# Optimization experiments

Hardware: AMD Instinct MI355X
Metric: run time of the kernel (lower is better)

The kernel has to match this reference:

```python
import jax, jax.numpy as jnp
import numpy as np

N_HEADS = 8

def setup_inputs() -> dict:
    key = jax.random.key(0)
    ks = jax.random.split(key, 8)
    N, D, H = 20000, 16, 256
    scale = np.float32(0.02)
    return {
        "h": jax.random.normal(ks[0], (N, H), dtype=jnp.float32),
        "attention_mask": jnp.zeros((N,), dtype=jnp.float32),
        "neighbor_idx": jax.random.randint(ks[1], (N, D), 0, N, dtype=jnp.int32),
        "Wq": jax.random.normal(ks[2], (H, H), dtype=jnp.float32) * scale,
        "bq": jnp.zeros((H,), dtype=jnp.float32),
        "Wk": jax.random.normal(ks[3], (H, H), dtype=jnp.float32) * scale,
        "bk": jnp.zeros((H,), dtype=jnp.float32),
        "Wv": jax.random.normal(ks[4], (H, H), dtype=jnp.float32) * scale,
        "bv": jnp.zeros((H,), dtype=jnp.float32),
    }

def reference(h, attention_mask, neighbor_idx, Wq, bq, Wk, bk, Wv, bv):
    N, H = h.shape
    nh = N_HEADS
    dh = H // nh
    inv_sqrt_dh = np.float32(1.0 / np.sqrt(dh))
    # query from each node's own state: [N, nh, dh]
    q = (h @ Wq.T + bq).reshape(N, nh, dh)
    # gather neighbor mailbox: [N, D, H]
    nb = h[neighbor_idx]
    k = (nb @ Wk.T + bk).reshape(N, -1, nh, dh)  # [N, D, nh, dh]
    v = (nb @ Wv.T + bv).reshape(N, -1, nh, dh)
    # scores: [N, nh, D]
    scores = jnp.einsum('nhd,nkhd->nhk', q, k) * inv_sqrt_dh
    # additive mask gathered from source nodes, broadcast over heads
    scores = scores + attention_mask[neighbor_idx][:, None, :]
    probs = jax.nn.softmax(scores, axis=-1)
    # dropout prob = 0.0 (eval) -> identity
    ctx = jnp.einsum('nhk,nkhd->nhd', probs, v).reshape(N, H)
    return ctx
```

## Files before the change

### kernel.cpp

```cpp
#include <hip/hip_runtime.h>
#include <hip/hip_fp16.h>
#include <math.h>

#define HDIM 256
#define DNEIGH 16

typedef __attribute__((ext_vector_type(8))) short short8;
typedef __attribute__((ext_vector_type(4))) float f32x4;

static __device__ __forceinline__ unsigned short f2bf(float f) {
    unsigned int u = __float_as_uint(f);
    unsigned int r = (u + 0x7fffu + ((u >> 16) & 1u)) >> 16;
    return (unsigned short)r;
}
static __device__ __forceinline__ float bf_lo(unsigned int u) {
    return __uint_as_float(u << 16);
}
static __device__ __forceinline__ float bf_hi(unsigned int u) {
    return __uint_as_float(u & 0xffff0000u);
}

#if __has_builtin(__builtin_amdgcn_cvt_pk_fp8_f32)
static __device__ __forceinline__ unsigned char f2fp8(float v) {
    int pk = __builtin_amdgcn_cvt_pk_fp8_f32(v, v, 0, false);
    return (unsigned char)(pk & 0xff);
}
#else
static __device__ __forceinline__ unsigned char f2fp8(float v) {
    unsigned short h = __half_as_ushort(__float2half(v * (1.0f / 256.0f)));
    unsigned short mag = h & 0x7fffu;
    mag = (unsigned short)((mag + 0x40u) >> 7);
    if (mag > 0x7f) mag = 0x7f;
    return (unsigned char)(((h >> 8) & 0x80u) | mag);
}
#endif

#if __has_builtin(__builtin_amdgcn_cvt_f32_fp8)
#define FP8D(u, i) __builtin_amdgcn_cvt_f32_fp8((u), (i))
#else
static __device__ __forceinline__ float fp8_byte_dec(unsigned int b) {
    unsigned int hb = ((b & 0x80u) << 8) | ((b & 0x7fu) << 7);
    return __half2float(__ushort_as_half((unsigned short)hb)) * 256.0f;
}
#define FP8D(u, i) fp8_byte_dec(((u) >> ((i) * 8)) & 0xffu)
#endif

static __device__ __forceinline__ void async_copy16(const void* g, void* l) {
    __builtin_amdgcn_global_load_lds(
        (const __attribute__((address_space(1))) unsigned int*)g,
        (__attribute__((address_space(3))) unsigned int*)l, 16, 0, 0);
}

__global__ __launch_bounds__(256) void cvt_kernel(
    const float* __restrict__ h,
    const float* __restrict__ wq, const float* __restrict__ wk, const float* __restrict__ wv,
    unsigned short* __restrict__ hb,
    unsigned short* __restrict__ wqb, unsigned short* __restrict__ wkb, unsigned short* __restrict__ wvb,
    int nh4)
{
    int i = blockIdx.x * 256 + threadIdx.x;
    const int total = nh4 + 3 * 16384;
    if (i >= total) return;
    const float4* src; unsigned short* dst; int off;
    if (i < nh4) { src = (const float4*)h; dst = hb; off = i; }
    else {
        int j = i - nh4; int s = j >> 14; off = j & 16383;
        src = (s == 0) ? (const float4*)wq : (s == 1) ? (const float4*)wk : (const float4*)wv;
        dst = (s == 0) ? wqb : (s == 1) ? wkb : wvb;
    }
    float4 v = src[off];
    ushort4 o;
    o.x = f2bf(v.x); o.y = f2bf(v.y); o.z = f2bf(v.z); o.w = f2bf(v.w);
    *(ushort4*)&dst[off * 4] = o;
}

__global__ __launch_bounds__(256, 1) void qkv_mfma_kernel(
    const unsigned short* __restrict__ hb,
    const unsigned short* __restrict__ Wqb,
    const unsigned short* __restrict__ Wkb,
    const unsigned short* __restrict__ Wvb,
    const float* __restrict__ bq, const float* __restrict__ bk, const float* __restrict__ bv,
    unsigned short* __restrict__ Qb, unsigned char* __restrict__ K8,
    unsigned short* __restrict__ Vb,
    int N)
{
    __shared__ unsigned short Ws[128 * 256];
    __shared__ unsigned short As[2][64 * 256];

    const int t = threadIdx.x;
    const int lane = t & 63;
    const int wid = t >> 6;
    const int wo = wid >> 1;
    const int wn2 = wid & 1;
    const int o0 = blockIdx.y * 128;
    const int sel = o0 >> 8;
    const int wrow0 = o0 & 255;

    const unsigned short* __restrict__ W = (sel == 0) ? Wqb : (sel == 1) ? Wkb : Wvb;
    const float* __restrict__ bias = (sel == 0) ? bq : (sel == 1) ? bk : bv;

    const int ntiles = (N + 63) >> 6;
    const int BX = gridDim.x;

    const int p = lane & 31;
    const int rhalf = lane >> 5;

#pragma unroll
    for (int r = 0; r < 16; ++r) {
        int lr = wid * 32 + r * 2 + rhalf;
        int c = (p & ~7) | ((p ^ lr) & 7);
        const unsigned short* gp = &W[(size_t)(wrow0 + lr) * 256 + c * 8];
        async_copy16(gp, &Ws[(wid * 32 + r * 2) * 256]);
    }
    {
        int g0 = blockIdx.x * 64;
#pragma unroll
        for (int r = 0; r < 8; ++r) {
            int lr = wid * 16 + r * 2 + rhalf;
            int c = (p & ~7) | ((p ^ lr) & 7);
            const unsigned short* gp = &hb[(size_t)(g0 + lr) * 256 + c * 8];
            async_copy16(gp, &As[0][(wid * 16 + r * 2) * 256]);
        }
    }
    __syncthreads();

    short8 af[8][4];
#pragma unroll
    for (int ks = 0; ks < 8; ++ks)
#pragma unroll
        for (int i = 0; i < 4; ++i) {
            int m = wo * 64 + i * 16 + (lane & 15);
            int c = ks * 4 + (lane >> 4);
            int pos = (c & ~7) | ((c ^ m) & 7);
            af[ks][i] = *(const short8*)&Ws[m * 256 + pos * 8];
        }

    const float qscale = 0.17677669529663688f;

    int tile = blockIdx.x;
    for (int it = 0; tile < ntiles; ++it, tile += BX) {
        int cur = it & 1;
        int nxt = tile + BX;
        if (nxt < ntiles) {
            int g0 = nxt * 64;
#pragma unroll
            for (int r = 0; r < 8; ++r) {
                int lr = wid * 16 + r * 2 + rhalf;
                int c = (p & ~7) | ((p ^ lr) & 7);
                const unsigned short* gp = &hb[(size_t)(g0 + lr) * 256 + c * 8];
                async_copy16(gp, &As[cur ^ 1][(wid * 16 + r * 2) * 256]);
            }
        }

        f32x4 acc[4][2] = {};
#pragma unroll
        for (int ks = 0; ks < 8; ++ks) {
            short8 bf[2];
#pragma unroll
            for (int j = 0; j < 2; ++j) {
                int n = wn2 * 32 + j * 16 + (lane & 15);
                int c = ks * 4 + (lane >> 4);
                int pos = (c & ~7) | ((c ^ n) & 7);
                bf[j] = *(const short8*)&As[cur][n * 256 + pos * 8];
            }
#pragma unroll
            for (int i = 0; i < 4; ++i)
#pragma unroll
                for (int j = 0; j < 2; ++j)
                    acc[i][j] = __builtin_amdgcn_mfma_f32_16x16x32_bf16(af[ks][i], bf[j], acc[i][j], 0, 0, 0);
        }

        int nodeb = tile * 64;
#pragma unroll
        for (int i = 0; i < 4; ++i) {
            int ch = wrow0 + wo * 64 + i * 16 + (lane >> 4) * 4;
            float4 b4 = *(const float4*)&bias[ch];
#pragma unroll
            for (int j = 0; j < 2; ++j) {
                int node = nodeb + wn2 * 32 + j * 16 + (lane & 15);
                if (node < N) {
                    float v0 = acc[i][j][0] + b4.x;
                    float v1 = acc[i][j][1] + b4.y;
                    float v2 = acc[i][j][2] + b4.z;
                    float v3 = acc[i][j][3] + b4.w;
                    if (sel == 0) {
                        ushort4 o;
                        o.x = f2bf(v0 * qscale); o.y = f2bf(v1 * qscale);
                        o.z = f2bf(v2 * qscale); o.w = f2bf(v3 * qscale);
                        *(ushort4*)&Qb[(size_t)node * HDIM + ch] = o;
                    } else if (sel == 1) {
                        uchar4 o;
                        o.x = f2fp8(v0); o.y = f2fp8(v1); o.z = f2fp8(v2); o.w = f2fp8(v3);
                        *(uchar4*)&K8[(size_t)node * HDIM + ch] = o;
                    } else {
                        ushort4 o;
                        o.x = f2bf(v0); o.y = f2bf(v1); o.z = f2bf(v2); o.w = f2bf(v3);
                        *(ushort4*)&Vb[(size_t)node * HDIM + ch] = o;
                    }
                }
            }
        }
        __syncthreads();
    }
}

__global__ __launch_bounds__(256) void attn4_kernel(
    const unsigned short* __restrict__ Qb,
    const unsigned char* __restrict__ K8,
    const unsigned short* __restrict__ Vb,
    const float* __restrict__ mask,
    const int* __restrict__ nidx,
    float* __restrict__ out,
    int N)
{
    const int w = threadIdx.x >> 6;
    const int lane = threadIdx.x & 63;
    const int n = blockIdx.x * 4 + w;
    if (n >= N) return;

    int idl = nidx[(size_t)n * DNEIGH + (lane & 15)];
    float mskl = mask[idl];

    unsigned int kreg[DNEIGH];
    uint2 vreg[DNEIGH];
#pragma unroll
    for (int d = 0; d < DNEIGH; ++d) {
        int id = __builtin_amdgcn_readlane(idl, d);
        kreg[d] = *(const unsigned int*)&K8[(size_t)id * HDIM + lane * 4];
        vreg[d] = *(const uint2*)&Vb[(size_t)id * HDIM + lane * 4];
    }

    uint2 qu = *(const uint2*)&Qb[(size_t)n * HDIM + lane * 4];
    const float q0 = bf_lo(qu.x), q1 = bf_hi(qu.x);
    const float q2 = bf_lo(qu.y), q3 = bf_hi(qu.y);

    float e[DNEIGH];
    float s = 0.f;
#pragma unroll
    for (int d = 0; d < DNEIGH; ++d) {
        float pdot = q0 * FP8D(kreg[d], 0) + q1 * FP8D(kreg[d], 1)
                   + q2 * FP8D(kreg[d], 2) + q3 * FP8D(kreg[d], 3);
        pdot += __shfl_xor(pdot, 1);
        pdot += __shfl_xor(pdot, 2);
        pdot += __shfl_xor(pdot, 4);
        float mk = __int_as_float(__builtin_amdgcn_readlane(__float_as_int(mskl), d));
        e[d] = __expf(pdot + mk);
        s += e[d];
    }
    float rs = 1.f / s;

    float4 acc = make_float4(0.f, 0.f, 0.f, 0.f);
#pragma unroll
    for (int d = 0; d < DNEIGH; ++d) {
        float wgt = e[d] * rs;
        acc.x += wgt * bf_lo(vreg[d].x);
        acc.y += wgt * bf_hi(vreg[d].x);
        acc.z += wgt * bf_lo(vreg[d].y);
        acc.w += wgt * bf_hi(vreg[d].y);
    }
    *(float4*)&out[(size_t)n * HDIM + lane * 4] = acc;
}

extern "C" void kernel_launch(void* const* d_in, const int* in_sizes, int n_in,
                              void* d_out, int out_size, void* d_ws, size_t ws_size,
                              hipStream_t stream)
{
    const float* h    = (const float*)d_in[0];
    const float* mask = (const float*)d_in[1];
    const int*   nidx = (const int*)d_in[2];
    const float* Wq   = (const float*)d_in[3];
    const float* bq   = (const float*)d_in[4];
    const float* Wk   = (const float*)d_in[5];
    const float* bk   = (const float*)d_in[6];
    const float* Wv   = (const float*)d_in[7];
    const float* bv   = (const float*)d_in[8];

    const int N = in_sizes[0] / HDIM;

    char* ws = (char*)d_ws;
    unsigned short* Qbp = (unsigned short*)ws; ws += (size_t)N * HDIM * 2;
    unsigned short* Vbp = (unsigned short*)ws; ws += (size_t)N * HDIM * 2;
    unsigned short* hbp = (unsigned short*)ws; ws += (size_t)N * HDIM * 2;
    unsigned char*  K8p = (unsigned char*)ws;  ws += (size_t)N * HDIM;
    unsigned short* Wqb = (unsigned short*)ws; ws += 65536 * 2;
    unsigned short* Wkb = (unsigned short*)ws; ws += 65536 * 2;
    unsigned short* Wvb = (unsigned short*)ws;

    const int nh4 = (N * HDIM) / 4;
    const int total = nh4 + 3 * 16384;
    cvt_kernel<<<(total + 255) / 256, 256, 0, stream>>>(h, Wq, Wk, Wv, hbp, Wqb, Wkb, Wvb, nh4);

    dim3 g1(42, 6);
    qkv_mfma_kernel<<<g1, 256, 0, stream>>>(hbp, Wqb, Wkb, Wvb, bq, bk, bv, Qbp, K8p, Vbp, N);

    attn4_kernel<<<(N + 3) / 4, 256, 0, stream>>>(Qbp, K8p, Vbp, mask, nidx, (float*)d_out, N);
}
```

Baseline: 137.5 us.

## Give each QKV block the full 256-channel weight slab and reuse LDS

Result: no change. 136.8 us (-0.5%).

```diff
diff --git a/kernel.cpp b/kernel.cpp
--- a/kernel.cpp
+++ b/kernel.cpp
@@ -84,62 +84,63 @@
     unsigned short* __restrict__ Vb,
     int N)
 {
-    __shared__ unsigned short Ws[128 * 256];
-    __shared__ unsigned short As[2][64 * 256];
+    __shared__ unsigned short LDSU[65536];
 
     const int t = threadIdx.x;
     const int lane = t & 63;
     const int wid = t >> 6;
-    const int wo = wid >> 1;
-    const int wn2 = wid & 1;
-    const int o0 = blockIdx.y * 128;
-    const int sel = o0 >> 8;
-    const int wrow0 = o0 & 255;
+    const int sel = blockIdx.y;
 
     const unsigned short* __restrict__ W = (sel == 0) ? Wqb : (sel == 1) ? Wkb : Wvb;
     const float* __restrict__ bias = (sel == 0) ? bq : (sel == 1) ? bk : bv;
 
+    const int p = lane & 31;
+    const int rhalf = lane >> 5;
+
+#pragma unroll
+    for (int r = 0; r < 32; ++r) {
+        int lr = wid * 64 + r * 2 + rhalf;
+        int c = (p & ~7) | ((p ^ lr) & 7);
+        async_copy16(&W[(size_t)lr * 256 + c * 8], &LDSU[(wid * 64 + r * 2) * 256]);
+    }
+    __syncthreads();
+
+    short8 af[8][4];
+#pragma unroll
+    for (int ks = 0; ks < 8; ++ks)
+#pragma unroll
+        for (int i = 0; i < 4; ++i) {
+            int m = wid * 64 + i * 16 + (lane & 15);
+            int c = ks * 4 + (lane >> 4);
+            int pos = (c & ~7) | ((c ^ m) & 7);
+            af[ks][i] = *(const short8*)&LDSU[m * 256 + pos * 8];
+        }
+    __syncthreads();
+
+    unsigned short* As0 = &LDSU[0];
+    unsigned short* As1 = &LDSU[16384];
+
     const int ntiles = (N + 63) >> 6;
     const int BX = gridDim.x;
-
-    const int p = lane & 31;
-    const int rhalf = lane >> 5;
-
-#pragma unroll
-    for (int r = 0; r < 16; ++r) {
-        int lr = wid * 32 + r * 2 + rhalf;
-        int c = (p & ~7) | ((p ^ lr) & 7);
-        const unsigned short* gp = &W[(size_t)(wrow0 + lr) * 256 + c * 8];
-        async_copy16(gp, &Ws[(wid * 32 + r * 2) * 256]);
-    }
+    int tile = blockIdx.x;
+
     {
-        int g0 = blockIdx.x * 64;
+        int g0 = tile * 64;
 #pragma unroll
         for (int r = 0; r < 8; ++r) {
             int lr = wid * 16 + r * 2 + rhalf;
             int c = (p & ~7) | ((p ^ lr) & 7);
-            const unsigned short* gp = &hb[(size_t)(g0 + lr) * 256 + c * 8];
-            async_copy16(gp, &As[0][(wid * 16 + r * 2) * 256]);
+            async_copy16(&hb[(size_t)(g0 + lr) * 256 + c * 8],
+                         &As0[(wid * 16 + r * 2) * 256]);
         }
     }
     __syncthreads();
 
-    short8 af[8][4];
-#pragma unroll
-    for (int ks = 0; ks < 8; ++ks)
-#pragma unroll
-        for (int i = 0; i < 4; ++i) {
-            int m = wo * 64 + i * 16 + (lane & 15);
-            int c = ks * 4 + (lane >> 4);
-            int pos = (c & ~7) | ((c ^ m) & 7);
-            af[ks][i] = *(const short8*)&Ws[m * 256 + pos * 8];
-        }
-
     const float qscale = 0.17677669529663688f;
 
-    int tile = blockIdx.x;
     for (int it = 0; tile < ntiles; ++it, tile += BX) {
-        int cur = it & 1;
+        unsigned short* curb = (it & 1) ? As1 : As0;
+        unsigned short* nxtb = (it & 1) ? As0 : As1;
         int nxt = tile + BX;
         if (nxt < ntiles) {
             int g0 = nxt * 64;
@@ -147,37 +148,37 @@
             for (int r = 0; r < 8; ++r) {
                 int lr = wid * 16 + r * 2 + rhalf;
                 int c = (p & ~7) | ((p ^ lr) & 7);
-                const unsigned short* gp = &hb[(size_t)(g0 + lr) * 256 + c * 8];
-                async_copy16(gp, &As[cur ^ 1][(wid * 16 + r * 2) * 256]);
+                async_copy16(&hb[(size_t)(g0 + lr) * 256 + c * 8],
+                             &nxtb[(wid * 16 + r * 2) * 256]);
             }
         }
 
-        f32x4 acc[4][2] = {};
+        f32x4 acc[4][4] = {};
 #pragma unroll
         for (int ks = 0; ks < 8; ++ks) {
-            short8 bf[2];
-#pragma unroll
-            for (int j = 0; j < 2; ++j) {
-                int n = wn2 * 32 + j * 16 + (lane & 15);
+            short8 bf[4];
+#pragma unroll
+            for (int j = 0; j < 4; ++j) {
+                int n = j * 16 + (lane & 15);
                 int c = ks * 4 + (lane >> 4);
                 int pos = (c & ~7) | ((c ^ n) & 7);
-                bf[j] = *(const short8*)&As[cur][n * 256 + pos * 8];
+                bf[j] = *(const short8*)&curb[n * 256 + pos * 8];
             }
 #pragma unroll
             for (int i = 0; i < 4; ++i)
 #pragma unroll
-                for (int j = 0; j < 2; ++j)
+                for (int j = 0; j < 4; ++j)
                     acc[i][j] = __builtin_amdgcn_mfma_f32_16x16x32_bf16(af[ks][i], bf[j], acc[i][j], 0, 0, 0);
         }
 
         int nodeb = tile * 64;
 #pragma unroll
         for (int i = 0; i < 4; ++i) {
-            int ch = wrow0 + wo * 64 + i * 16 + (lane >> 4) * 4;
+            int ch = wid * 64 + i * 16 + (lane >> 4) * 4;
             float4 b4 = *(const float4*)&bias[ch];
 #pragma unroll
-            for (int j = 0; j < 2; ++j) {
-                int node = nodeb + wn2 * 32 + j * 16 + (lane & 15);
+            for (int j = 0; j < 4; ++j) {
+                int node = nodeb + j * 16 + (lane & 15);
                 if (node < N) {
                     float v0 = acc[i][j][0] + b4.x;
                     float v1 = acc[i][j][1] + b4.y;
@@ -290,7 +291,7 @@
     const int total = nh4 + 3 * 16384;
     cvt_kernel<<<(total + 255) / 256, 256, 0, stream>>>(h, Wq, Wk, Wv, hbp, Wqb, Wkb, Wvb, nh4);
 
-    dim3 g1(42, 6);
+    dim3 g1(85, 3);
     qkv_mfma_kernel<<<g1, 256, 0, stream>>>(hbp, Wqb, Wkb, Wvb, bq, bk, bv, Qbp, K8p, Vbp, N);
 
     attn4_kernel<<<(N + 3) / 4, 256, 0, stream>>>(Qbp, K8p, Vbp, mask, nidx, (float*)d_out, N);
```
